# Optimization experiments

Measured on AMD Instinct MI355X. Metric: run time of the kernel, lower is better.

The kernel has to match this reference:

```python
import jax, jax.numpy as jnp
import numpy as np

D_MODEL = 768
N_HEADS = 12


def setup_inputs() -> dict:
    key = jax.random.key(0)
    ks = jax.random.split(key, 9)
    s = 1.0 / np.sqrt(D_MODEL)
    return {
        "x": jax.random.normal(ks[0], (1, 4096, D_MODEL), dtype=jnp.float32),
        "w_q": jax.random.normal(ks[1], (D_MODEL, D_MODEL), dtype=jnp.float32) * s,
        "b_q": jnp.zeros((D_MODEL,), dtype=jnp.float32),
        "w_k": jax.random.normal(ks[2], (D_MODEL, D_MODEL), dtype=jnp.float32) * s,
        "b_k": jnp.zeros((D_MODEL,), dtype=jnp.float32),
        "w_v": jax.random.normal(ks[3], (D_MODEL, D_MODEL), dtype=jnp.float32) * s,
        "b_v": jnp.zeros((D_MODEL,), dtype=jnp.float32),
        "w_o": jax.random.normal(ks[4], (D_MODEL, D_MODEL), dtype=jnp.float32) * s,
        "b_o": jnp.zeros((D_MODEL,), dtype=jnp.float32),
    }


def reference(x, w_q, b_q, w_k, b_k, w_v, b_v, w_o, b_o):
    b, l, dm = x.shape
    h = N_HEADS
    dk = dm // h
    # projections ([b,l,dm] @ [dm,dm]) then split heads -> [b,h,l,dk]
    def proj(w, bias):
        y = x @ w + bias
        return y.reshape(b, l, h, dk).transpose(0, 2, 1, 3)
    q = proj(w_q, b_q)
    k = proj(w_k, b_k)
    v = proj(w_v, b_v)
    scale = jnp.asarray(dk, x.dtype) ** 0.5
    scores = jnp.einsum("bhqd,bhkd->bhqk", q, k)  # [b,h,l,l]
    causal = jnp.triu(jnp.ones((l, l), dtype=bool), k=1)
    scores = jnp.where(causal, -jnp.inf, scores)
    weights = jax.nn.softmax(scores / scale, axis=-1)
    heads = jnp.einsum("bhqk,bhkd->bhqd", weights, v)  # [b,h,l,dk]
    heads = heads.transpose(0, 2, 1, 3).reshape(b, l, dm)
    return heads @ w_o + b_o
```

## Files before the change

### kernel.cpp

```cpp
#include <hip/hip_runtime.h>

#define L_SEQ 4096
#define DMODEL 768
#define NH 12
#define DK 64

typedef __bf16 bf16;
typedef __bf16 bf16x8 __attribute__((ext_vector_type(8)));
typedef __bf16 bf16x4 __attribute__((ext_vector_type(4)));
typedef float f32x4 __attribute__((ext_vector_type(4)));

#define QSCALE 0.1803368801111204f
#define DEFER_THR 8.0f

__global__ __launch_bounds__(256) void prep_kernel(
    const float* __restrict__ x,
    const float* __restrict__ w_q, const float* __restrict__ w_k,
    const float* __restrict__ w_v, const float* __restrict__ w_o,
    bf16* __restrict__ xb, bf16* __restrict__ wqt, bf16* __restrict__ wkt,
    bf16* __restrict__ wvt, bf16* __restrict__ wot)
{
    const int bid = blockIdx.x;
    const int t = threadIdx.x;
    if (bid < 576) {
        __shared__ bf16 Ls[64][72];
        const int mat = bid / 144;
        const int tile = bid % 144;
        const int k0 = (tile / 12) * 64;
        const int c0 = (tile % 12) * 64;
        const float* W = mat == 0 ? w_q : mat == 1 ? w_k : mat == 2 ? w_v : w_o;
        bf16* WT = mat == 0 ? wqt : mat == 1 ? wkt : mat == 2 ? wvt : wot;
        #pragma unroll
        for (int p = 0; p < 4; ++p) {
            int id = t + p * 256;
            int r = id >> 4, c4 = id & 15;
            float4 v = *(const float4*)(W + (size_t)(k0 + r) * DMODEL + c0 + c4 * 4);
            bf16x4 b; b[0] = (bf16)v.x; b[1] = (bf16)v.y; b[2] = (bf16)v.z; b[3] = (bf16)v.w;
            *(bf16x4*)&Ls[r][c4 * 4] = b;
        }
        __syncthreads();
        #pragma unroll
        for (int p = 0; p < 2; ++p) {
            int id = t + p * 256;
            int crow = id >> 3, kc = id & 7;
            bf16x8 o;
            #pragma unroll
            for (int e = 0; e < 8; ++e) o[e] = Ls[kc * 8 + e][crow];
            *(bf16x8*)(WT + (size_t)(c0 + crow) * DMODEL + k0 + kc * 8) = o;
        }
    } else {
        const size_t base = (size_t)(bid - 576) * 4096;
        #pragma unroll
        for (int p = 0; p < 4; ++p) {
            size_t idx = base + (size_t)(t + p * 256) * 4;
            float4 v = *(const float4*)(x + idx);
            bf16x4 b; b[0] = (bf16)v.x; b[1] = (bf16)v.y; b[2] = (bf16)v.z; b[3] = (bf16)v.w;
            *(bf16x4*)(xb + idx) = b;
        }
    }
}

__global__ __launch_bounds__(256) void proj_kernel(
    const bf16* __restrict__ xb,
    const bf16* __restrict__ wqt, const bf16* __restrict__ wkt, const bf16* __restrict__ wvt,
    const float* __restrict__ b_q, const float* __restrict__ b_k, const float* __restrict__ b_v,
    bf16* __restrict__ qbuf, bf16* __restrict__ kbuf, bf16* __restrict__ vt)
{
    __shared__ bf16 As[128][72];
    __shared__ bf16 Bs[64][72];
    const int t = threadIdx.x;
    const int w = t >> 6, l = t & 63;
    const int lg = l >> 4, lr = l & 15;

    if (blockIdx.x < 768) {
        const int bn = blockIdx.x % 24;
        const int bm = blockIdx.x / 24;
        const int m0 = bm * 128;
        const int gn0 = bn * 64;
        const int sel = gn0 / DMODEL;
        const int c0 = gn0 % DMODEL;
        const bf16* WT = sel ? wkt : wqt;
        const float* bias = sel ? b_k : b_q;
        bf16* dst = sel ? kbuf : qbuf;
        const float scale = sel ? 1.0f : QSCALE;

        f32x4 acc[2][4];
        #pragma unroll
        for (int i = 0; i < 2; i++)
            #pragma unroll
            for (int j = 0; j < 4; j++) acc[i][j] = (f32x4){0.f, 0.f, 0.f, 0.f};

        for (int kk = 0; kk < DMODEL; kk += 64) {
            #pragma unroll
            for (int p = 0; p < 4; ++p) {
                int id = t + p * 256;
                int row = id >> 3, ch = id & 7;
                *(bf16x8*)&As[row][ch * 8] =
                    *(const bf16x8*)(xb + (size_t)(m0 + row) * DMODEL + kk + ch * 8);
            }
            #pragma unroll
            for (int p = 0; p < 2; ++p) {
                int id = t + p * 256;
                int n = id >> 3, ch = id & 7;
                *(bf16x8*)&Bs[n][ch * 8] =
                    *(const bf16x8*)(WT + (size_t)(c0 + n) * DMODEL + kk + ch * 8);
            }
            __syncthreads();
            #pragma unroll
            for (int ks = 0; ks < 2; ++ks) {
                bf16x8 a[2], bfr[4];
                #pragma unroll
                for (int i = 0; i < 2; i++) a[i] = *(const bf16x8*)&As[w * 32 + i * 16 + lr][ks * 32 + lg * 8];
                #pragma unroll
                for (int j = 0; j < 4; j++) bfr[j] = *(const bf16x8*)&Bs[j * 16 + lr][ks * 32 + lg * 8];
                #pragma unroll
                for (int i = 0; i < 2; i++)
                    #pragma unroll
                    for (int j = 0; j < 4; j++)
                        acc[i][j] = __builtin_amdgcn_mfma_f32_16x16x32_bf16(a[i], bfr[j], acc[i][j], 0, 0, 0);
            }
            __syncthreads();
        }
        #pragma unroll
        for (int i = 0; i < 2; i++) {
            #pragma unroll
            for (int j = 0; j < 4; j++) {
                int c = c0 + j * 16 + lr;
                int h = c >> 6, d = c & 63;
                float bb = bias[c];
                #pragma unroll
                for (int r = 0; r < 4; r++) {
                    int m = m0 + w * 32 + i * 16 + lg * 4 + r;
                    float v = (acc[i][j][r] + bb) * scale;
                    dst[((size_t)h * L_SEQ + m) * DK + d] = (bf16)v;
                }
            }
        }
    } else {
        const int bid = blockIdx.x - 768;
        const int bc = bid % 12;
        const int bmm = bid / 12;
        const int c0 = bc * 64;
        const int mm0 = bmm * 128;

        f32x4 acc[8];
        #pragma unroll
        for (int j = 0; j < 8; j++) acc[j] = (f32x4){0.f, 0.f, 0.f, 0.f};

        for (int kk = 0; kk < DMODEL; kk += 64) {
            #pragma unroll
            for (int p = 0; p < 4; ++p) {
                int id = t + p * 256;
                int row = id >> 3, ch = id & 7;
                *(bf16x8*)&As[row][ch * 8] =
                    *(const bf16x8*)(xb + (size_t)(mm0 + row) * DMODEL + kk + ch * 8);
            }
            #pragma unroll
            for (int p = 0; p < 2; ++p) {
                int id = t + p * 256;
                int n = id >> 3, ch = id & 7;
                *(bf16x8*)&Bs[n][ch * 8] =
                    *(const bf16x8*)(wvt + (size_t)(c0 + n) * DMODEL + kk + ch * 8);
            }
            __syncthreads();
            #pragma unroll
            for (int ks = 0; ks < 2; ++ks) {
                bf16x8 a = *(const bf16x8*)&Bs[w * 16 + lr][ks * 32 + lg * 8];
                #pragma unroll
                for (int j = 0; j < 8; j++) {
                    bf16x8 b = *(const bf16x8*)&As[j * 16 + lr][ks * 32 + lg * 8];
                    acc[j] = __builtin_amdgcn_mfma_f32_16x16x32_bf16(a, b, acc[j], 0, 0, 0);
                }
            }
            __syncthreads();
        }
        #pragma unroll
        for (int j = 0; j < 8; j++) {
            int m = mm0 + j * 16 + lr;
            #pragma unroll
            for (int r = 0; r < 4; r++) {
                int c = c0 + w * 16 + lg * 4 + r;
                float v = acc[j][r] + b_v[c];
                vt[(size_t)c * L_SEQ + m] = (bf16)v;
            }
        }
    }
}

__global__ __launch_bounds__(512) void attn_kernel(
    const bf16* __restrict__ qbuf, const bf16* __restrict__ kbuf,
    const bf16* __restrict__ vt, bf16* __restrict__ obuf)
{
    __shared__ __align__(16) char lds[49152];

    const int bid = blockIdx.x;
    const int h  = bid % NH;
    const int qt = 63 - (bid / NH);
    const int q0 = qt * 64;
    const int nt = qt + 1;
    const int nit = (nt + 1) >> 1;

    const int t = threadIdx.x;
    const int w = t >> 6;
    const int g = w >> 2;
    const int wg = w & 3;
    const int l = t & 63;
    const int lg = l >> 4, lr = l & 15;
    const int tg = t & 255;
    const int sw = (lr & 7) << 4;

    char* Kbase = lds + (size_t)g * 8192;
    char* Vbase = lds + 16384 + (size_t)g * 8192;
    char* Pbase = lds + 32768 + (size_t)w * 2048;
    float* mergeAcc = (float*)lds;
    float* mergeM   = (float*)(lds + 22528);

    const size_t qrow = (size_t)h * L_SEQ + q0 + wg * 16 + lr;
    const bf16x8 qa0 = *(const bf16x8*)(qbuf + qrow * DK + 0  + lg * 8);
    const bf16x8 qa1 = *(const bf16x8*)(qbuf + qrow * DK + 32 + lg * 8);

    bf16x8 ones;
    #pragma unroll
    for (int e = 0; e < 8; ++e) ones[e] = (bf16)1.0f;

    f32x4 acc[4];
    #pragma unroll
    for (int j = 0; j < 4; j++) acc[j] = (f32x4){0.f, 0.f, 0.f, 0.f};
    f32x4 acc_sum = (f32x4){0.f, 0.f, 0.f, 0.f};
    float run_m = -1e30f;

    const bf16* kb_base = kbuf + (size_t)h * L_SEQ * DK;
    const bf16* vt_base = vt + (size_t)h * DK * L_SEQ;

    bf16x8 k8[2], v8[2];
    if (g < nt) {
        #pragma unroll
        for (int p = 0; p < 2; ++p) {
            int id = tg + p * 256;
            int row = id >> 3, ch = id & 7;
            k8[p] = *(const bf16x8*)(kb_base + (size_t)(g * 64 + row) * DK + ch * 8);
            v8[p] = *(const bf16x8*)(vt_base + (size_t)row * L_SEQ + g * 64 + ch * 8);
        }
    }

    for (int it = 0; it < nit; ++it) {
        const int cur = 2 * it + g;
        const bool active = (cur < nt);
        __syncthreads();
        if (active) {
            #pragma unroll
            for (int p = 0; p < 2; ++p) {
                int id = tg + p * 256;
                int row = id >> 3, ch = id & 7;
                int so = (ch * 16) ^ ((row & 7) << 4);
                *(bf16x8*)(Kbase + row * 128 + so) = k8[p];
                *(bf16x8*)(Vbase + row * 128 + so) = v8[p];
            }
        }
        __syncthreads();
        const int nxt = cur + 2;
        if (nxt < nt) {
            #pragma unroll
            for (int p = 0; p < 2; ++p) {
                int id = tg + p * 256;
                int row = id >> 3, ch = id & 7;
                k8[p] = *(const bf16x8*)(kb_base + (size_t)(nxt * 64 + row) * DK + ch * 8);
                v8[p] = *(const bf16x8*)(vt_base + (size_t)row * L_SEQ + nxt * 64 + ch * 8);
            }
        }
        if (active) {
            f32x4 s[4];
            #pragma unroll
            for (int j = 0; j < 4; j++) s[j] = (f32x4){0.f, 0.f, 0.f, 0.f};
            __builtin_amdgcn_s_setprio(1);
            #pragma unroll
            for (int dh = 0; dh < 2; ++dh) {
                const bf16x8 qa = dh ? qa1 : qa0;
                #pragma unroll
                for (int j = 0; j < 4; j++) {
                    bf16x8 kb = *(const bf16x8*)(Kbase + (j * 16 + lr) * 128 + ((dh * 64 + lg * 16) ^ sw));
                    s[j] = __builtin_amdgcn_mfma_f32_16x16x32_bf16(kb, qa, s[j], 0, 0, 0);
                }
            }
            __builtin_amdgcn_s_setprio(0);
            if (cur == qt) {
                const int qoff = wg * 16 + lr;
                #pragma unroll
                for (int j = 0; j < 4; j++)
                    #pragma unroll
                    for (int r = 0; r < 4; r++)
                        if (j * 16 + lg * 4 + r > qoff) s[j][r] = -3e30f;
            }
            float m0 = fmaxf(fmaxf(s[0][0], s[0][1]), s[0][2]);
            float m1 = fmaxf(fmaxf(s[0][3], s[1][0]), s[1][1]);
            float m2 = fmaxf(fmaxf(s[1][2], s[1][3]), s[2][0]);
            float m3 = fmaxf(fmaxf(s[2][1], s[2][2]), s[2][3]);
            float m4 = fmaxf(fmaxf(s[3][0], s[3][1]), s[3][2]);
            float t1 = fmaxf(fmaxf(m0, m1), m2);
            float t2 = fmaxf(fmaxf(m3, m4), s[3][3]);
            float mx = fmaxf(t1, t2);
            mx = fmaxf(mx, __shfl_xor(mx, 16));
            mx = fmaxf(mx, __shfl_xor(mx, 32));
            if (!__all(mx <= run_m + DEFER_THR)) {
                const float nm = fmaxf(run_m, mx);
                const float scq = exp2f(run_m - nm);
                run_m = nm;
                float sc0 = __shfl(scq, lg * 4 + 0);
                float sc1 = __shfl(scq, lg * 4 + 1);
                float sc2 = __shfl(scq, lg * 4 + 2);
                float sc3 = __shfl(scq, lg * 4 + 3);
                #pragma unroll
                for (int jd = 0; jd < 4; jd++) {
                    acc[jd][0] *= sc0; acc[jd][1] *= sc1;
                    acc[jd][2] *= sc2; acc[jd][3] *= sc3;
                }
                acc_sum[0] *= sc0; acc_sum[1] *= sc1;
                acc_sum[2] *= sc2; acc_sum[3] *= sc3;
            }
            #pragma unroll
            for (int j = 0; j < 4; j++)
                #pragma unroll
                for (int r = 0; r < 4; r++) s[j][r] = exp2f(s[j][r] - run_m);
            #pragma unroll
            for (int j = 0; j < 4; j++) {
                bf16x4 pk;
                pk[0] = (bf16)s[j][0]; pk[1] = (bf16)s[j][1];
                pk[2] = (bf16)s[j][2]; pk[3] = (bf16)s[j][3];
                *(bf16x4*)(Pbase + lr * 128 + ((j * 32 + lg * 8) ^ sw)) = pk;
            }
            __builtin_amdgcn_s_setprio(1);
            #pragma unroll
            for (int dh = 0; dh < 2; ++dh) {
                bf16x8 pa = *(const bf16x8*)(Pbase + lr * 128 + ((dh * 64 + lg * 16) ^ sw));
                acc_sum = __builtin_amdgcn_mfma_f32_16x16x32_bf16(pa, ones, acc_sum, 0, 0, 0);
                #pragma unroll
                for (int jd = 0; jd < 4; jd++) {
                    bf16x8 vb = *(const bf16x8*)(Vbase + (jd * 16 + lr) * 128 + ((dh * 64 + lg * 16) ^ sw));
                    acc[jd] = __builtin_amdgcn_mfma_f32_16x16x32_bf16(pa, vb, acc[jd], 0, 0, 0);
                }
            }
            __builtin_amdgcn_s_setprio(0);
        }
    }

    __syncthreads();
    if (g == 1) {
        float* base = mergeAcc + (size_t)(wg * 64 + l) * 21;
        #pragma unroll
        for (int jd = 0; jd < 4; jd++)
            #pragma unroll
            for (int r = 0; r < 4; r++) base[jd * 4 + r] = acc[jd][r];
        #pragma unroll
        for (int r = 0; r < 4; r++) base[16 + r] = acc_sum[r];
        mergeM[wg * 64 + l] = run_m;
    }
    __syncthreads();
    if (g == 0) {
        const float* base = mergeAcc + (size_t)(wg * 64 + l) * 21;
        const float mB = mergeM[wg * 64 + l];
        const float mF = fmaxf(run_m, mB);
        const float sa = exp2f(run_m - mF);
        const float sb = exp2f(mB - mF);
        float a4[4], b4[4];
        #pragma unroll
        for (int r = 0; r < 4; r++) {
            a4[r] = __shfl(sa, lg * 4 + r);
            b4[r] = __shfl(sb, lg * 4 + r);
        }
        #pragma unroll
        for (int jd = 0; jd < 4; jd++) {
            #pragma unroll
            for (int r = 0; r < 4; r++) {
                float denom = acc_sum[r] * a4[r] + base[16 + r] * b4[r];
                float v = acc[jd][r] * a4[r] + base[jd * 4 + r] * b4[r];
                int m = q0 + wg * 16 + lg * 4 + r;
                obuf[(size_t)m * DMODEL + h * DK + jd * 16 + lr] = (bf16)(v / denom);
            }
        }
    }
}

__global__ __launch_bounds__(256) void out_proj_kernel(
    const bf16* __restrict__ obuf, const bf16* __restrict__ wot,
    const float* __restrict__ b_o, float* __restrict__ out)
{
    __shared__ bf16 As[128][72];
    __shared__ bf16 Bts[64][72];
    const int bn = blockIdx.x % 12;
    const int bm = blockIdx.x / 12;
    const int m0 = bm * 128, c0 = bn * 64;
    const int t = threadIdx.x;
    const int w = t >> 6, l = t & 63, lg = l >> 4, lr = l & 15;

    f32x4 acc[2][4];
    #pragma unroll
    for (int i = 0; i < 2; i++)
        #pragma unroll
        for (int j = 0; j < 4; j++) acc[i][j] = (f32x4){0.f, 0.f, 0.f, 0.f};

    for (int kk = 0; kk < DMODEL; kk += 64) {
        #pragma unroll
        for (int p = 0; p < 4; ++p) {
            int id = t + p * 256;
            int row = id >> 3, ch = id & 7;
            *(bf16x8*)&As[row][ch * 8] =
                *(const bf16x8*)(obuf + (size_t)(m0 + row) * DMODEL + kk + ch * 8);
        }
        #pragma unroll
        for (int p = 0; p < 2; ++p) {
            int id = t + p * 256;
            int n = id >> 3, ch = id & 7;
            *(bf16x8*)&Bts[n][ch * 8] =
                *(const bf16x8*)(wot + (size_t)(c0 + n) * DMODEL + kk + ch * 8);
        }
        __syncthreads();
        #pragma unroll
        for (int ks = 0; ks < 2; ++ks) {
            bf16x8 a[2], bfr[4];
            #pragma unroll
            for (int i = 0; i < 2; i++) a[i] = *(const bf16x8*)&As[w * 32 + i * 16 + lr][ks * 32 + lg * 8];
            #pragma unroll
            for (int j = 0; j < 4; j++) bfr[j] = *(const bf16x8*)&Bts[j * 16 + lr][ks * 32 + lg * 8];
            #pragma unroll
            for (int i = 0; i < 2; i++)
                #pragma unroll
                for (int j = 0; j < 4; j++)
                    acc[i][j] = __builtin_amdgcn_mfma_f32_16x16x32_bf16(a[i], bfr[j], acc[i][j], 0, 0, 0);
        }
        __syncthreads();
    }
    #pragma unroll
    for (int i = 0; i < 2; i++) {
        #pragma unroll
        for (int j = 0; j < 4; j++) {
            int c = c0 + j * 16 + lr;
            float bb = b_o[c];
            #pragma unroll
            for (int r = 0; r < 4; r++) {
                int m = m0 + w * 32 + i * 16 + lg * 4 + r;
                out[(size_t)m * DMODEL + c] = acc[i][j][r] + bb;
            }
        }
    }
}

extern "C" void kernel_launch(void* const* d_in, const int* in_sizes, int n_in,
                              void* d_out, int out_size, void* d_ws, size_t ws_size,
                              hipStream_t stream) {
    const float* x   = (const float*)d_in[0];
    const float* w_q = (const float*)d_in[1];
    const float* b_q = (const float*)d_in[2];
    const float* w_k = (const float*)d_in[3];
    const float* b_k = (const float*)d_in[4];
    const float* w_v = (const float*)d_in[5];
    const float* b_v = (const float*)d_in[6];
    const float* w_o = (const float*)d_in[7];
    const float* b_o = (const float*)d_in[8];
    float* out = (float*)d_out;

    char* ws = (char*)d_ws;
    const size_t SZ = (size_t)NH * L_SEQ * DK * sizeof(bf16);
    const size_t WTSZ = (size_t)DMODEL * DMODEL * sizeof(bf16);
    bf16* qbuf = (bf16*)(ws);
    bf16* kbuf = (bf16*)(ws + SZ);
    bf16* vt   = (bf16*)(ws + 2 * SZ);
    bf16* obuf = (bf16*)(ws + 3 * SZ);
    bf16* xb   = (bf16*)(ws + 4 * SZ);
    bf16* wqt  = (bf16*)(ws + 5 * SZ);
    bf16* wkt  = (bf16*)(ws + 5 * SZ + WTSZ);
    bf16* wvt  = (bf16*)(ws + 5 * SZ + 2 * WTSZ);
    bf16* wot  = (bf16*)(ws + 5 * SZ + 3 * WTSZ);

    prep_kernel<<<dim3(1344), dim3(256), 0, stream>>>(x, w_q, w_k, w_v, w_o, xb, wqt, wkt, wvt, wot);
    proj_kernel<<<dim3(1152), dim3(256), 0, stream>>>(xb, wqt, wkt, wvt, b_q, b_k, b_v, qbuf, kbuf, vt);
    attn_kernel<<<dim3(768), dim3(512), 0, stream>>>(qbuf, kbuf, vt, obuf);
    out_proj_kernel<<<dim3(384), dim3(256), 0, stream>>>(obuf, wot, b_o, out);
}
```

Before: 115.3 us.

## Async double-buffered K/V loads into LDS and keep P in registers

The projection kernel now writes K and V^T in pre-swizzled 64-row tile layouts, so the attention kernel can copy each tile straight into LDS with global_load_lds. The copy is double-buffered, which removes the register round-trip and one barrier per iteration. The P matrix is no longer staged through LDS: the exp results stay in registers and feed 16x16x16 MFMAs, with matching 4-element V reads. The cost is a larger LDS footprint (64KB) and twice as many smaller MFMA instructions.

Measured after the change: 119.1 us. 3.3% more time.

```diff
diff --git a/kernel.cpp b/kernel.cpp
--- a/kernel.cpp
+++ b/kernel.cpp
@@ -8,10 +8,17 @@
 typedef __bf16 bf16;
 typedef __bf16 bf16x8 __attribute__((ext_vector_type(8)));
 typedef __bf16 bf16x4 __attribute__((ext_vector_type(4)));
+typedef short short4v __attribute__((ext_vector_type(4)));
 typedef float f32x4 __attribute__((ext_vector_type(4)));
 
 #define QSCALE 0.1803368801111204f
 #define DEFER_THR 8.0f
+
+__device__ __forceinline__ void gload16(const void* g, void* l) {
+    __builtin_amdgcn_global_load_lds(
+        (const __attribute__((address_space(1))) unsigned int*)g,
+        (__attribute__((address_space(3))) unsigned int*)l, 16, 0, 0);
+}
 
 __global__ __launch_bounds__(256) void prep_kernel(
     const float* __restrict__ x,
@@ -81,7 +88,6 @@
         const int c0 = gn0 % DMODEL;
         const bf16* WT = sel ? wkt : wqt;
         const float* bias = sel ? b_k : b_q;
-        bf16* dst = sel ? kbuf : qbuf;
         const float scale = sel ? 1.0f : QSCALE;
 
         f32x4 acc[2][4];
@@ -132,7 +138,13 @@
                 for (int r = 0; r < 4; r++) {
                     int m = m0 + w * 32 + i * 16 + lg * 4 + r;
                     float v = (acc[i][j][r] + bb) * scale;
-                    dst[((size_t)h * L_SEQ + m) * DK + d] = (bf16)v;
+                    if (sel == 0) {
+                        qbuf[((size_t)h * L_SEQ + m) * DK + d] = (bf16)v;
+                    } else {
+                        size_t idx = (size_t)h * L_SEQ * DK + (size_t)(m >> 6) * 4096
+                                   + (size_t)(m & 63) * 64 + (((d >> 3) ^ (m & 7)) << 3) + (d & 7);
+                        kbuf[idx] = (bf16)v;
+                    }
                 }
             }
         }
@@ -181,7 +193,9 @@
             for (int r = 0; r < 4; r++) {
                 int c = c0 + w * 16 + lg * 4 + r;
                 float v = acc[j][r] + b_v[c];
-                vt[(size_t)c * L_SEQ + m] = (bf16)v;
+                size_t idx = (size_t)(c >> 6) * DK * L_SEQ + (size_t)(m >> 6) * 4096
+                           + (size_t)(c & 63) * 64 + ((((m >> 3) & 7) ^ (c & 7)) << 3) + (m & 7);
+                vt[idx] = (bf16)v;
             }
         }
     }
@@ -191,7 +205,7 @@
     const bf16* __restrict__ qbuf, const bf16* __restrict__ kbuf,
     const bf16* __restrict__ vt, bf16* __restrict__ obuf)
 {
-    __shared__ __align__(16) char lds[49152];
+    __shared__ __align__(16) char lds[65536];
 
     const int bid = blockIdx.x;
     const int h  = bid % NH;
@@ -209,9 +223,6 @@
     const int tg = t & 255;
     const int sw = (lr & 7) << 4;
 
-    char* Kbase = lds + (size_t)g * 8192;
-    char* Vbase = lds + 16384 + (size_t)g * 8192;
-    char* Pbase = lds + 32768 + (size_t)w * 2048;
     float* mergeAcc = (float*)lds;
     float* mergeM   = (float*)(lds + 22528);
 
@@ -219,9 +230,11 @@
     const bf16x8 qa0 = *(const bf16x8*)(qbuf + qrow * DK + 0  + lg * 8);
     const bf16x8 qa1 = *(const bf16x8*)(qbuf + qrow * DK + 32 + lg * 8);
 
-    bf16x8 ones;
+    bf16x4 ones_b;
     #pragma unroll
-    for (int e = 0; e < 8; ++e) ones[e] = (bf16)1.0f;
+    for (int e = 0; e < 4; ++e) ones_b[e] = (bf16)1.0f;
+    union { bf16x4 b; short4v s; } ocv; ocv.b = ones_b;
+    const short4v ones_s = ocv.s;
 
     f32x4 acc[4];
     #pragma unroll
@@ -232,43 +245,42 @@
     const bf16* kb_base = kbuf + (size_t)h * L_SEQ * DK;
     const bf16* vt_base = vt + (size_t)h * DK * L_SEQ;
 
-    bf16x8 k8[2], v8[2];
     if (g < nt) {
+        const bf16* kg = kb_base + (size_t)g * 4096;
+        const bf16* vg = vt_base + (size_t)g * 4096;
+        char* kl = lds + (size_t)(g << 1) * 8192;
+        char* vl = lds + 32768 + (size_t)(g << 1) * 8192;
         #pragma unroll
         for (int p = 0; p < 2; ++p) {
             int id = tg + p * 256;
-            int row = id >> 3, ch = id & 7;
-            k8[p] = *(const bf16x8*)(kb_base + (size_t)(g * 64 + row) * DK + ch * 8);
-            v8[p] = *(const bf16x8*)(vt_base + (size_t)row * L_SEQ + g * 64 + ch * 8);
+            gload16(kg + id * 8, kl + id * 16);
+            gload16(vg + id * 8, vl + id * 16);
         }
     }
 
     for (int it = 0; it < nit; ++it) {
         const int cur = 2 * it + g;
         const bool active = (cur < nt);
-        __syncthreads();
-        if (active) {
+        const int b = it & 1;
+        asm volatile("s_waitcnt vmcnt(0)" ::: "memory");
+        __builtin_amdgcn_sched_barrier(0);
+        __builtin_amdgcn_s_barrier();
+        const int nxt = cur + 2;
+        if (nxt < nt) {
+            const bf16* kg = kb_base + (size_t)nxt * 4096;
+            const bf16* vg = vt_base + (size_t)nxt * 4096;
+            char* kl = lds + (size_t)((g << 1) | (b ^ 1)) * 8192;
+            char* vl = lds + 32768 + (size_t)((g << 1) | (b ^ 1)) * 8192;
             #pragma unroll
             for (int p = 0; p < 2; ++p) {
                 int id = tg + p * 256;
-                int row = id >> 3, ch = id & 7;
-                int so = (ch * 16) ^ ((row & 7) << 4);
-                *(bf16x8*)(Kbase + row * 128 + so) = k8[p];
-                *(bf16x8*)(Vbase + row * 128 + so) = v8[p];
-            }
-        }
-        __syncthreads();
-        const int nxt = cur + 2;
-        if (nxt < nt) {
-            #pragma unroll
-            for (int p = 0; p < 2; ++p) {
-                int id = tg + p * 256;
-                int row = id >> 3, ch = id & 7;
-                k8[p] = *(const bf16x8*)(kb_base + (size_t)(nxt * 64 + row) * DK + ch * 8);
-                v8[p] = *(const bf16x8*)(vt_base + (size_t)row * L_SEQ + nxt * 64 + ch * 8);
+                gload16(kg + id * 8, kl + id * 16);
+                gload16(vg + id * 8, vl + id * 16);
             }
         }
         if (active) {
+            char* Kbase = lds + (size_t)((g << 1) | b) * 8192;
+            char* Vbase = lds + 32768 + (size_t)((g << 1) | b) * 8192;
             f32x4 s[4];
             #pragma unroll
             for (int j = 0; j < 4; j++) s[j] = (f32x4){0.f, 0.f, 0.f, 0.f};
@@ -317,26 +329,24 @@
                 acc_sum[0] *= sc0; acc_sum[1] *= sc1;
                 acc_sum[2] *= sc2; acc_sum[3] *= sc3;
             }
-            #pragma unroll
-            for (int j = 0; j < 4; j++)
-                #pragma unroll
-                for (int r = 0; r < 4; r++) s[j][r] = exp2f(s[j][r] - run_m);
+            short4v pa[4];
             #pragma unroll
             for (int j = 0; j < 4; j++) {
                 bf16x4 pk;
-                pk[0] = (bf16)s[j][0]; pk[1] = (bf16)s[j][1];
-                pk[2] = (bf16)s[j][2]; pk[3] = (bf16)s[j][3];
-                *(bf16x4*)(Pbase + lr * 128 + ((j * 32 + lg * 8) ^ sw)) = pk;
+                #pragma unroll
+                for (int r = 0; r < 4; r++) pk[r] = (bf16)exp2f(s[j][r] - run_m);
+                union { bf16x4 b; short4v s; } cv; cv.b = pk;
+                pa[j] = cv.s;
             }
             __builtin_amdgcn_s_setprio(1);
             #pragma unroll
-            for (int dh = 0; dh < 2; ++dh) {
-                bf16x8 pa = *(const bf16x8*)(Pbase + lr * 128 + ((dh * 64 + lg * 16) ^ sw));
-                acc_sum = __builtin_amdgcn_mfma_f32_16x16x32_bf16(pa, ones, acc_sum, 0, 0, 0);
+            for (int j = 0; j < 4; j++) {
+                acc_sum = __builtin_amdgcn_mfma_f32_16x16x16bf16_1k(pa[j], ones_s, acc_sum, 0, 0, 0);
                 #pragma unroll
                 for (int jd = 0; jd < 4; jd++) {
-                    bf16x8 vb = *(const bf16x8*)(Vbase + (jd * 16 + lr) * 128 + ((dh * 64 + lg * 16) ^ sw));
-                    acc[jd] = __builtin_amdgcn_mfma_f32_16x16x32_bf16(pa, vb, acc[jd], 0, 0, 0);
+                    short4v vb = *(const short4v*)(Vbase + (jd * 16 + lr) * 128
+                                   + ((((j << 1) | (lg >> 1)) << 4) ^ sw) + ((lg & 1) << 3));
+                    acc[jd] = __builtin_amdgcn_mfma_f32_16x16x16bf16_1k(pa[j], vb, acc[jd], 0, 0, 0);
                 }
             }
             __builtin_amdgcn_s_setprio(0);
```
